# Kernel tuning notes

Hardware: AMD Instinct MI355X
Metric: run time of the kernel (lower is better)

The kernel has to match this reference:

```python
import jax, jax.numpy as jnp
import numpy as np

SCALES = (1, 3, 6)
PRECISION = 10  # pywt default: 2**10 samples of psi on [-5, 5]


def _gaus1_filters():
    """Replicates pywt.cwt's integrated-wavelet filters for wavelet='gaus1'.

    pywt: psi, x = wavelet.wavefun(10); int_psi = cumsum(psi)*step; per scale a:
    j = arange(a*(x[-1]-x[0])+1)/(a*step) -> int indices; filter = int_psi[j][::-1];
    conv = np.convolve(data, filter). np.convolve flips its kernel, so the
    equivalent cross-correlation kernel (lax.conv semantics) is int_psi[j].
    """
    x = np.linspace(-5.0, 5.0, 2 ** PRECISION)
    step = x[1] - x[0]
    psi = -2.0 * x * np.exp(-x ** 2) / (np.pi / 2.0) ** 0.25
    int_psi = np.cumsum(psi) * step
    filts = []
    for a in SCALES:
        j = (np.arange(a * (x[-1] - x[0]) + 1) / (a * step)).astype(np.int64)
        j = j[j < int_psi.size]
        filts.append(int_psi[j].astype(np.float32))  # correlation kernel
    return filts

_FILTS = _gaus1_filters()


def setup_inputs() -> dict:
    key = jax.random.key(0)
    x = jax.random.normal(key, (32, 4096, 64), dtype=jnp.float32)
    return {"x": x}


def reference(x):
    B, S, C = x.shape
    sig = jnp.transpose(x, (0, 2, 1)).reshape(B * C, 1, S)  # [B*C, 1, S]
    outs = []
    for a, f in zip(SCALES, _FILTS):
        L = f.shape[0]
        k = jnp.asarray(f).reshape(1, 1, L)
        # full convolution (np.convolve): pad L-1 both sides
        conv = jax.lax.conv_general_dilated(
            sig, k, window_strides=(1,), padding=[(L - 1, L - 1)],
            dimension_numbers=("NCH", "OIH", "NCH"))  # [B*C, 1, S+L-1]
        coef = -np.sqrt(a).astype(np.float32) * jnp.diff(conv, axis=-1)  # [B*C,1,S+L-2]
        d = (coef.shape[-1] - S) / 2.0
        coef = coef[..., int(np.floor(d)): coef.shape[-1] - int(np.ceil(d))]  # [B*C,1,S]
        outs.append(coef)
    out = jnp.concatenate(outs, axis=1).reshape(B, C, len(SCALES), S)
    return jnp.transpose(out, (0, 2, 3, 1))  # [B, 3, S, C]
```

## Files before the change

kernel.cpp:

```cpp
#include <hip/hip_runtime.h>
#include <math.h>

#define S_LEN  4096
#define NCH    64
#define TILE_S 64
#define RPT    8
#define TY     8
#define NQ     32
#define NQS    33
#define WQ     18
#define WLEN   72


constexpr double cexp_(double v) {
  const double LN2 = 0.6931471805599453;
  double t = v / LN2;
  int k = (int)t;
  if (t < 0.0 && (double)k != t) --k;
  double r = v - (double)k * LN2;
  double term = 1.0, sum = 1.0;
  for (int n = 1; n <= 22; ++n) { term *= r / (double)n; sum += term; }
  while (k > 0) { sum *= 2.0; --k; }
  while (k < 0) { sum *= 0.5; ++k; }
  return sum;
}
constexpr double csqrt_(double a) {
  double y = a > 1.0 ? a : 1.0;
  for (int i = 0; i < 64; ++i) y = 0.5 * (y + a / y);
  return y;
}
struct Wt { float w6[62]; float w3[32]; float w1[12]; };
constexpr Wt make_weights() {
  Wt w{};
  double ip[1024] = {};
  const double delta = 10.0 / 1023.0;
  const double step  = (-5.0 + delta) + 5.0;
  const double cn    = csqrt_(csqrt_(1.5707963267948966));
  double s = 0.0;
  for (int i = 0; i < 1024; ++i) {
    const double xi  = (i == 1023) ? 5.0 : ((double)i * delta - 5.0);
    const double psi = (-2.0 * xi) * cexp_(-(xi * xi)) / cn;
    s += psi;
    ip[i] = s * step;
  }
  const int as_[3] = {6, 3, 1};
  const int lf_[3] = {61, 31, 11};
  for (int si = 0; si < 3; ++si) {
    const double denom = (double)as_[si] * step;
    const float  sqa   = (float)csqrt_((double)as_[si]);
    const int    lf    = lf_[si];
    for (int t = 0; t <= lf; ++t) {
      float km1 = 0.f, kt = 0.f;
      if (t >= 1)      km1 = (float)ip[(long)(((double)(t - 1)) / denom)];
      if (t <= lf - 1) kt  = (float)ip[(long)(((double)t) / denom)];
      const float val = -sqa * (km1 - kt);
      if (si == 0) w.w6[t] = val; else if (si == 1) w.w3[t] = val; else w.w1[t] = val;
    }
  }
  return w;
}
constexpr Wt CW = make_weights();
template <int T> constexpr float W6 = CW.w6[T];
template <int T> constexpr float W3 = CW.w3[T];
template <int T> constexpr float W1 = CW.w1[T];

template <int T, int R>
struct FmaR {
  static __device__ __forceinline__ void run(const float (&win)[WLEN],
                                             float (&a6)[RPT], float (&a3)[RPT],
                                             float (&a1)[RPT]) {
    a6[R] = fmaf(W6<T>, win[T + R + 1], a6[R]);
    if constexpr (T >= 15 && T <= 46) a3[R] = fmaf(W3<T - 15>, win[T + R + 1], a3[R]);
    if constexpr (T >= 25 && T <= 36) a1[R] = fmaf(W1<T - 25>, win[T + R + 1], a1[R]);
    FmaR<T, R + 1>::run(win, a6, a3, a1);
  }
};
template <int T>
struct FmaR<T, RPT> {
  static __device__ __forceinline__ void run(const float (&)[WLEN],
                                             float (&)[RPT], float (&)[RPT], float (&)[RPT]) {}
};

template <int Q>
static __device__ __forceinline__ void load_quad(const float* __restrict__ colbase, int q0,
                                                 float (&win)[WLEN]) {
  const float4 v = *(const float4*)(colbase + ((q0 + Q) << 2));
  win[4 * Q + 0] = v.x; win[4 * Q + 1] = v.y; win[4 * Q + 2] = v.z; win[4 * Q + 3] = v.w;
}

template <int Q>
struct Burst {
  static __device__ __forceinline__ void run(const float* __restrict__ colbase, int q0,
                                             float (&win)[WLEN]) {
    load_quad<Q>(colbase, q0, win);
    Burst<Q + 1>::run(colbase, q0, win);
  }
};
template <>
struct Burst<WQ> {
  static __device__ __forceinline__ void run(const float* __restrict__, int, float (&)[WLEN]) {}
};

template <int T>
struct Step {
  static __device__ __forceinline__ void run(float (&win)[WLEN], float (&a6)[RPT],
                                             float (&a3)[RPT], float (&a1)[RPT]) {
    FmaR<T, 0>::run(win, a6, a3, a1);
    Step<T + 1>::run(win, a6, a3, a1);
  }
};
template <>
struct Step<62> {
  static __device__ __forceinline__ void run(float (&)[WLEN], float (&)[RPT],
                                             float (&)[RPT], float (&)[RPT]) {}
};

template <int R>
struct Store {
  static __device__ __forceinline__ void run(float* __restrict__ o1, float* __restrict__ o3,
                                             float* __restrict__ o6, const float (&a6)[RPT],
                                             const float (&a3)[RPT], const float (&a1)[RPT]) {
    o1[(size_t)R * NCH] = a1[R];
    o3[(size_t)R * NCH] = a3[R];
    o6[(size_t)R * NCH] = a6[R];
    Store<R + 1>::run(o1, o3, o6, a6, a3, a1);
  }
};
template <>
struct Store<RPT> {
  static __device__ __forceinline__ void run(float* __restrict__, float* __restrict__,
                                             float* __restrict__, const float (&)[RPT],
                                             const float (&)[RPT], const float (&)[RPT]) {}
};

template <int R>
struct Zero {
  static __device__ __forceinline__ void run(float (&a6)[RPT], float (&a3)[RPT], float (&a1)[RPT]) {
    a6[R] = 0.f; a3[R] = 0.f; a1[R] = 0.f;
    Zero<R + 1>::run(a6, a3, a1);
  }
};
template <>
struct Zero<RPT> {
  static __device__ __forceinline__ void run(float (&)[RPT], float (&)[RPT], float (&)[RPT]) {}
};

__global__ __launch_bounds__(512, 4)
void cwt_main(const float* __restrict__ x, float* __restrict__ out) {
  __shared__ __align__(16) float lds[NCH * NQS * 4];

  const int c  = threadIdx.x;
  const int ty = threadIdx.y;

  const int hw = blockIdx.x;
  const int wg = ((hw & 7) << 8) + (hw >> 3);
  const int sx = wg & 63;
  const int b  = wg >> 6;
  const int s0 = sx * TILE_S;
  const int ROW0 = s0 - 32;

  const float* __restrict__ xb = x + (size_t)b * S_LEN * NCH;

  {
    float pg[4][4];
    #pragma unroll
    for (int k = 0; k < 4; ++k) {
      #pragma unroll
      for (int j = 0; j < 4; ++j) {
        const int row = ROW0 + 16 * ty + 4 * k + j;
        float v = 0.f;
        if ((unsigned)row < (unsigned)S_LEN) v = xb[(size_t)row * NCH + c];
        pg[k][j] = v;
      }
    }
    #pragma unroll
    for (int k = 0; k < 4; ++k) {
      const int q = 4 * ty + k;
      *(float4*)&lds[c * (NQS * 4) + (q << 2)] =
          make_float4(pg[k][0], pg[k][1], pg[k][2], pg[k][3]);
    }
  }
  __syncthreads();

  const float* __restrict__ colbase = &lds[c * (NQS * 4)];
  const int q0 = 2 * ty;

  float win[WLEN];
  float a6[RPT], a3[RPT], a1[RPT];
  Zero<0>::run(a6, a3, a1);
  Burst<0>::run(colbase, q0, win);
  __builtin_amdgcn_sched_barrier(0);
  Step<0>::run(win, a6, a3, a1);

  const int srow = s0 + RPT * ty;
  float* o1 = out + (((size_t)b * 3 + 0) * S_LEN + srow) * NCH + c;
  float* o3 = out + (((size_t)b * 3 + 1) * S_LEN + srow) * NCH + c;
  float* o6 = out + (((size_t)b * 3 + 2) * S_LEN + srow) * NCH + c;
  Store<0>::run(o1, o3, o6, a6, a3, a1);
}

extern "C" void kernel_launch(void* const* d_in, const int* in_sizes, int n_in,
                              void* d_out, int out_size, void* d_ws, size_t ws_size,
                              hipStream_t stream) {
  (void)n_in; (void)out_size; (void)d_ws; (void)ws_size;
  const float* x = (const float*)d_in[0];
  float* out = (float*)d_out;
  const int B = in_sizes[0] / (S_LEN * NCH);

  const int nblk = (S_LEN / TILE_S) * B;
  dim3 grid(nblk);
  dim3 block(NCH, TY);
  hipLaunchKernelGGL(cwt_main, grid, block, 0, stream, x, out);
}
```

Baseline: 134.6 us.

## Use row-major LDS tile with float4 global loads and stream rows through register window

Replaces the transposed, padded column-major LDS layout with a row-major tile filled by coalesced float4 global loads. Each thread now computes one output row at a time, loading one new LDS element per row into its sliding window instead of keeping 24 accumulators live. Launch bounds rise to 6 waves per SIMD to raise occupancy. The trade is many scalar LDS reads in place of vectorised float4 reads, and less instruction-level parallelism per row.

```diff
diff --git a/kernel.cpp b/kernel.cpp
--- a/kernel.cpp
+++ b/kernel.cpp
@@ -6,10 +6,8 @@
 #define TILE_S 64
 #define RPT    8
 #define TY     8
-#define NQ     32
-#define NQS    33
-#define WQ     18
-#define WLEN   72
+#define NROWS  128
+#define WLEN   70
 
 
 constexpr double cexp_(double v) {
@@ -64,93 +62,62 @@
 template <int T> constexpr float W3 = CW.w3[T];
 template <int T> constexpr float W1 = CW.w1[T];
 
-template <int T, int R>
-struct FmaR {
-  static __device__ __forceinline__ void run(const float (&win)[WLEN],
-                                             float (&a6)[RPT], float (&a3)[RPT],
-                                             float (&a1)[RPT]) {
-    a6[R] = fmaf(W6<T>, win[T + R + 1], a6[R]);
-    if constexpr (T >= 15 && T <= 46) a3[R] = fmaf(W3<T - 15>, win[T + R + 1], a3[R]);
-    if constexpr (T >= 25 && T <= 36) a1[R] = fmaf(W1<T - 25>, win[T + R + 1], a1[R]);
-    FmaR<T, R + 1>::run(win, a6, a3, a1);
-  }
-};
-template <int T>
-struct FmaR<T, RPT> {
-  static __device__ __forceinline__ void run(const float (&)[WLEN],
-                                             float (&)[RPT], float (&)[RPT], float (&)[RPT]) {}
-};
-
-template <int Q>
-static __device__ __forceinline__ void load_quad(const float* __restrict__ colbase, int q0,
-                                                 float (&win)[WLEN]) {
-  const float4 v = *(const float4*)(colbase + ((q0 + Q) << 2));
-  win[4 * Q + 0] = v.x; win[4 * Q + 1] = v.y; win[4 * Q + 2] = v.z; win[4 * Q + 3] = v.w;
-}
-
-template <int Q>
-struct Burst {
-  static __device__ __forceinline__ void run(const float* __restrict__ colbase, int q0,
+template <int K>
+struct PreW {
+  static __device__ __forceinline__ void run(const float* __restrict__ colbase,
                                              float (&win)[WLEN]) {
-    load_quad<Q>(colbase, q0, win);
-    Burst<Q + 1>::run(colbase, q0, win);
+    win[K] = colbase[K * NCH];
+    PreW<K + 1>::run(colbase, win);
   }
 };
 template <>
-struct Burst<WQ> {
-  static __device__ __forceinline__ void run(const float* __restrict__, int, float (&)[WLEN]) {}
+struct PreW<63> {
+  static __device__ __forceinline__ void run(const float* __restrict__, float (&)[WLEN]) {}
 };
 
-template <int T>
-struct Step {
-  static __device__ __forceinline__ void run(float (&win)[WLEN], float (&a6)[RPT],
-                                             float (&a3)[RPT], float (&a1)[RPT]) {
-    FmaR<T, 0>::run(win, a6, a3, a1);
-    Step<T + 1>::run(win, a6, a3, a1);
+template <int R, int T>
+struct Tap {
+  static __device__ __forceinline__ void run(const float (&win)[WLEN], float& a6,
+                                             float& a3, float& a1) {
+    a6 = fmaf(W6<T>, win[T + R + 1], a6);
+    if constexpr (T >= 15 && T <= 46) a3 = fmaf(W3<T - 15>, win[T + R + 1], a3);
+    if constexpr (T >= 25 && T <= 36) a1 = fmaf(W1<T - 25>, win[T + R + 1], a1);
+    Tap<R, T + 1>::run(win, a6, a3, a1);
+  }
+};
+template <int R>
+struct Tap<R, 62> {
+  static __device__ __forceinline__ void run(const float (&)[WLEN], float&, float&, float&) {}
+};
+
+template <int R>
+struct Row {
+  static __device__ __forceinline__ void run(const float* __restrict__ colbase,
+                                             float (&win)[WLEN], float* __restrict__ o1,
+                                             float* __restrict__ o3, float* __restrict__ o6) {
+    if constexpr (R > 0) win[R + 62] = colbase[(R + 62) * NCH];
+    float a6 = 0.f, a3 = 0.f, a1 = 0.f;
+    Tap<R, 0>::run(win, a6, a3, a1);
+    o1[(size_t)R * NCH] = a1;
+    o3[(size_t)R * NCH] = a3;
+    o6[(size_t)R * NCH] = a6;
+    Row<R + 1>::run(colbase, win, o1, o3, o6);
   }
 };
 template <>
-struct Step<62> {
-  static __device__ __forceinline__ void run(float (&)[WLEN], float (&)[RPT],
-                                             float (&)[RPT], float (&)[RPT]) {}
+struct Row<RPT> {
+  static __device__ __forceinline__ void run(const float* __restrict__, float (&)[WLEN],
+                                             float* __restrict__, float* __restrict__,
+                                             float* __restrict__) {}
 };
 
-template <int R>
-struct Store {
-  static __device__ __forceinline__ void run(float* __restrict__ o1, float* __restrict__ o3,
-                                             float* __restrict__ o6, const float (&a6)[RPT],
-                                             const float (&a3)[RPT], const float (&a1)[RPT]) {
-    o1[(size_t)R * NCH] = a1[R];
-    o3[(size_t)R * NCH] = a3[R];
-    o6[(size_t)R * NCH] = a6[R];
-    Store<R + 1>::run(o1, o3, o6, a6, a3, a1);
-  }
-};
-template <>
-struct Store<RPT> {
-  static __device__ __forceinline__ void run(float* __restrict__, float* __restrict__,
-                                             float* __restrict__, const float (&)[RPT],
-                                             const float (&)[RPT], const float (&)[RPT]) {}
-};
-
-template <int R>
-struct Zero {
-  static __device__ __forceinline__ void run(float (&a6)[RPT], float (&a3)[RPT], float (&a1)[RPT]) {
-    a6[R] = 0.f; a3[R] = 0.f; a1[R] = 0.f;
-    Zero<R + 1>::run(a6, a3, a1);
-  }
-};
-template <>
-struct Zero<RPT> {
-  static __device__ __forceinline__ void run(float (&)[RPT], float (&)[RPT], float (&)[RPT]) {}
-};
-
-__global__ __launch_bounds__(512, 4)
+__global__ __launch_bounds__(512, 6)
 void cwt_main(const float* __restrict__ x, float* __restrict__ out) {
-  __shared__ __align__(16) float lds[NCH * NQS * 4];
+  __shared__ __align__(16) float lds[NROWS * NCH];
 
   const int c  = threadIdx.x;
   const int ty = threadIdx.y;
+  const int tid = ty * 64 + c;
 
   const int hw = blockIdx.x;
   const int wg = ((hw & 7) << 8) + (hw >> 3);
@@ -161,42 +128,29 @@
 
   const float* __restrict__ xb = x + (size_t)b * S_LEN * NCH;
 
-  {
-    float pg[4][4];
-    #pragma unroll
-    for (int k = 0; k < 4; ++k) {
-      #pragma unroll
-      for (int j = 0; j < 4; ++j) {
-        const int row = ROW0 + 16 * ty + 4 * k + j;
-        float v = 0.f;
-        if ((unsigned)row < (unsigned)S_LEN) v = xb[(size_t)row * NCH + c];
-        pg[k][j] = v;
-      }
-    }
-    #pragma unroll
-    for (int k = 0; k < 4; ++k) {
-      const int q = 4 * ty + k;
-      *(float4*)&lds[c * (NQS * 4) + (q << 2)] =
-          make_float4(pg[k][0], pg[k][1], pg[k][2], pg[k][3]);
-    }
+  #pragma unroll
+  for (int i = 0; i < 4; ++i) {
+    const int slot = tid + i * 512;
+    const int row  = slot >> 4, q = slot & 15;
+    const int grow = ROW0 + row;
+    float4 v = make_float4(0.f, 0.f, 0.f, 0.f);
+    if ((unsigned)grow < (unsigned)S_LEN)
+      v = *(const float4*)(xb + ((size_t)grow * NCH + (q << 2)));
+    *(float4*)&lds[row * NCH + (q << 2)] = v;
   }
   __syncthreads();
 
-  const float* __restrict__ colbase = &lds[c * (NQS * 4)];
-  const int q0 = 2 * ty;
+  const float* __restrict__ colbase = &lds[(RPT * ty) * NCH + c];
 
   float win[WLEN];
-  float a6[RPT], a3[RPT], a1[RPT];
-  Zero<0>::run(a6, a3, a1);
-  Burst<0>::run(colbase, q0, win);
-  __builtin_amdgcn_sched_barrier(0);
-  Step<0>::run(win, a6, a3, a1);
+  PreW<1>::run(colbase, win);
 
   const int srow = s0 + RPT * ty;
   float* o1 = out + (((size_t)b * 3 + 0) * S_LEN + srow) * NCH + c;
   float* o3 = out + (((size_t)b * 3 + 1) * S_LEN + srow) * NCH + c;
   float* o6 = out + (((size_t)b * 3 + 2) * S_LEN + srow) * NCH + c;
-  Store<0>::run(o1, o3, o6, a6, a3, a1);
+
+  Row<0>::run(colbase, win, o1, o3, o6);
 }
 
 extern "C" void kernel_launch(void* const* d_in, const int* in_sizes, int n_in,
```

Measured after the change: 136.1 us. About the same (+1.2%).
